# Kernel optimization log

Measured on AMD Instinct MI355X. Metric: run time of the kernel, lower is better.

The kernel has to match this reference:

```python
import jax, jax.numpy as jnp
import numpy as np

B, S, D_IN, D_OUT, H = 4, 2048, 2048, 2048, 16
HD = D_OUT // H  # head_dim = 128


def setup_inputs() -> dict:
    key = jax.random.key(0)
    ks = jax.random.split(key, 5)
    s = 0.02
    return {
        "x": jax.random.normal(ks[0], (B, S, D_IN), dtype=jnp.float32),
        "W_q": jax.random.normal(ks[1], (D_IN, D_OUT), dtype=jnp.float32) * s,
        "W_k": jax.random.normal(ks[2], (D_IN, D_OUT), dtype=jnp.float32) * s,
        "W_v": jax.random.normal(ks[3], (D_IN, D_OUT), dtype=jnp.float32) * s,
        "W_o": jax.random.normal(ks[4], (D_OUT, D_OUT), dtype=jnp.float32) * s,
        "b_o": jnp.zeros((D_OUT,), dtype=jnp.float32),
    }


def reference(x, W_q, W_k, W_v, W_o, b_o):
    b, n, _ = x.shape
    # projections (qkv_bias=False), split into heads: [b, h, n, hd]
    q = (x @ W_q).reshape(b, n, H, HD).transpose(0, 2, 1, 3)
    k = (x @ W_k).reshape(b, n, H, HD).transpose(0, 2, 1, 3)
    v = (x @ W_v).reshape(b, n, H, HD).transpose(0, 2, 1, 3)
    # scores [b, h, n, n], causal mask (triu, diagonal=1) applied BEFORE scaling
    scores = jnp.einsum("bhqd,bhkd->bhqk", q, k)
    causal = jnp.triu(jnp.ones((n, n), dtype=bool), k=1)
    scores = jnp.where(causal, -jnp.inf, scores)
    scale = jnp.asarray(HD, scores.dtype) ** 0.5
    attn = jax.nn.softmax(scores / scale, axis=-1)
    ctx = jnp.einsum("bhqk,bhkd->bhqd", attn, v)
    ctx = ctx.transpose(0, 2, 1, 3).reshape(b, n, D_OUT)
    return ctx @ W_o + b_o
```

## Files before the change

### kernel.cpp

```cpp
#include <hip/hip_runtime.h>
#include <hip/hip_bf16.h>
#include <math.h>

#define H_   16
#define S_   2048
#define D_   2048
#define HD_  128
#define B_   4
#define M_   8192

typedef __attribute__((ext_vector_type(8))) short short8;
typedef __attribute__((ext_vector_type(4))) short short4v;
typedef __attribute__((ext_vector_type(4))) float f32x4;

__device__ __forceinline__ short f2bf(float f) {
  unsigned u = __float_as_uint(f);
  u += 0x7fff + ((u >> 16) & 1);
  return (short)(u >> 16);
}

__device__ __forceinline__ unsigned pk2(float a, float b) {
  __hip_bfloat162 h = __float22bfloat162_rn(float2{a, b});
  union { __hip_bfloat162 h2; unsigned u; } c;
  c.h2 = h;
  return c.u;
}

__device__ __forceinline__ void async16(const void* g, void* l) {
  __builtin_amdgcn_global_load_lds(
      (const __attribute__((address_space(1))) void*)g,
      (__attribute__((address_space(3))) void*)l, 16, 0, 0);
}

__global__ void k_cvtx(const float* __restrict__ x, short* __restrict__ o, int n4) {
  const int i = blockIdx.x * 256 + threadIdx.x;
  if (i >= n4) return;
  const float4 f = ((const float4*)x)[i];
  short4v s;
  s.x = f2bf(f.x); s.y = f2bf(f.y); s.z = f2bf(f.z); s.w = f2bf(f.w);
  ((short4v*)o)[i] = s;
}

__global__ void k_wtrans(const float* __restrict__ W, short* __restrict__ Wt) {
  __shared__ float t[32][33];
  const int n0 = blockIdx.x << 5, k0 = blockIdx.y << 5;
  const int tc = threadIdx.x & 31, tr = threadIdx.x >> 5;
#pragma unroll
  for (int i = 0; i < 32; i += 8)
    t[tr + i][tc] = W[(size_t)(k0 + tr + i) * D_ + n0 + tc];
  __syncthreads();
#pragma unroll
  for (int i = 0; i < 32; i += 8)
    Wt[(size_t)(n0 + tr + i) * D_ + k0 + tc] = f2bf(t[tc][tr + i]);
}

template <int MODE>
__global__ __launch_bounds__(256)
void k_gemm_bt(const short* __restrict__ A, const short* __restrict__ Bt,
               void* __restrict__ C0, void* __restrict__ C1, void* __restrict__ C2,
               const float* __restrict__ bias, int M, int N, int K) {
  __shared__ __align__(16) short As[2][128 * 32];
  __shared__ __align__(16) short Bs[2][128 * 32];
  const int tid = threadIdx.x;
  const int lane = tid & 63;
  const int wave = tid >> 6;
  const int ln = lane & 15, lq = lane >> 4;
  const int bm = blockIdx.y << 7;
  const int bn = blockIdx.x << 7;
  const int wm = (wave >> 1) << 6;
  const int wn = (wave & 1) << 6;

  f32x4 acc[4][4];
#pragma unroll
  for (int i = 0; i < 4; i++)
#pragma unroll
    for (int j = 0; j < 4; j++) acc[i][j] = (f32x4)0.0f;

  const int srow = wave * 16 + (lane >> 2);
  const int scol = (lane & 3) * 8;
  const short* Ag = A  + (size_t)(bm + srow) * K + scol;
  const short* Bg = Bt + (size_t)(bn + srow) * K + scol;
  const int w16 = wave * 16 * 32;
  const int w16b = (64 + wave * 16) * 32;

  const int niter = K >> 5;
  async16(Ag, &As[0][w16]);
  async16(Ag + (size_t)64 * K, &As[0][w16b]);
  async16(Bg, &Bs[0][w16]);
  async16(Bg + (size_t)64 * K, &Bs[0][w16b]);

#pragma unroll 1
  for (int it = 0; it < niter; it++) {
    const int cur = it & 1;
    __syncthreads();
    if (it + 1 < niter) {
      const int k0 = (it + 1) << 5;
      async16(Ag + k0, &As[cur ^ 1][w16]);
      async16(Ag + (size_t)64 * K + k0, &As[cur ^ 1][w16b]);
      async16(Bg + k0, &Bs[cur ^ 1][w16]);
      async16(Bg + (size_t)64 * K + k0, &Bs[cur ^ 1][w16b]);
    }

    short8 af[4], bf[4];
#pragma unroll
    for (int i = 0; i < 4; i++)
      af[i] = *(const short8*)(&As[cur][(wm + i * 16 + ln) * 32 + lq * 8]);
#pragma unroll
    for (int i = 0; i < 4; i++)
      bf[i] = *(const short8*)(&Bs[cur][(wn + i * 16 + ln) * 32 + lq * 8]);
#pragma unroll
    for (int mi = 0; mi < 4; mi++)
#pragma unroll
      for (int ni = 0; ni < 4; ni++)
        acc[mi][ni] = __builtin_amdgcn_mfma_f32_16x16x32_bf16(
            af[mi], bf[ni], acc[mi][ni], 0, 0, 0);
  }

  if (MODE == 0) {
    const int proj = bn >> 11;
    const int cb = bn & 2047;
    if (proj < 2) {
      short* C = (short*)(proj == 0 ? C0 : C1);
#pragma unroll
      for (int mi = 0; mi < 4; mi++)
#pragma unroll
        for (int ni = 0; ni < 4; ni++) {
          const int col = cb + wn + ni * 16 + ln;
          const int h = col >> 7, d = col & 127;
#pragma unroll
          for (int r = 0; r < 4; r++) {
            const int row = bm + wm + mi * 16 + lq * 4 + r;
            const int bb = row >> 11, s = row & 2047;
            C[((size_t)((bb * H_ + h) * S_ + s)) * HD_ + d] = f2bf(acc[mi][ni][r]);
          }
        }
    } else {
      short* C = (short*)C2;
#pragma unroll
      for (int mi = 0; mi < 4; mi++)
#pragma unroll
        for (int ni = 0; ni < 4; ni++) {
          const int col = cb + wn + ni * 16 + ln;
          const int h = col >> 7, d = col & 127;
          const int row0 = bm + wm + mi * 16 + lq * 4;
          const int bb = row0 >> 11, s = row0 & 2047;
          short4v pk;
#pragma unroll
          for (int r = 0; r < 4; r++) pk[r] = f2bf(acc[mi][ni][r]);
          *(short4v*)(C + ((size_t)((bb * H_ + h) * HD_ + d)) * S_ + s) = pk;
        }
    }
  } else {
    float* C = (float*)C0;
#pragma unroll
    for (int mi = 0; mi < 4; mi++)
#pragma unroll
      for (int ni = 0; ni < 4; ni++) {
        const int col = bn + wn + ni * 16 + ln;
        const float bv = bias[col];
#pragma unroll
        for (int r = 0; r < 4; r++) {
          const int row = bm + wm + mi * 16 + lq * 4 + r;
          C[(size_t)row * N + col] = acc[mi][ni][r] + bv;
        }
      }
  }
}

__global__ __launch_bounds__(256)
void k_flash(const short* __restrict__ Q, const short* __restrict__ K,
             const short* __restrict__ Vt, short* __restrict__ ctx) {
  __shared__ __align__(16) short Ks[2][64 * 128];
  __shared__ __align__(16) short Vs[2][128 * 64];
  __shared__ __align__(16) short Ps[4 * 32 * 64];

  const int tid = threadIdx.x, lane = tid & 63, w = tid >> 6;
  const int ln = lane & 15, lq = lane >> 4;
  const int bh = blockIdx.x & 63;
  const int pr = blockIdx.x >> 6;
  const int b = bh >> 4, h = bh & 15;
  const short* Qp = Q  + (size_t)bh * S_ * HD_;
  const short* Kp = K  + (size_t)bh * S_ * HD_;
  const short* Vp = Vt + (size_t)bh * HD_ * S_;

  const float sc = 0.08838834764831845f * 1.4426950408889634f;
  const int lx = ln & 7;

  int koff[4], voff[4];
#pragma unroll
  for (int it = 0; it < 4; it++) {
    const int kr = w * 16 + it * 4 + (lane >> 4);
    koff[it] = kr * HD_ + (((lane & 15) ^ (kr & 7)) * 8);
    const int vr = w * 32 + it * 8 + (lane >> 3);
    voff[it] = vr * S_ + (((lane & 7) ^ (vr & 7)) * 8);
  }

#pragma unroll 1
  for (int pass = 0; pass < 2; pass++) {
    const int qb = pass ? (15 - pr) : pr;
    const int q0 = qb << 7;
    const int qw = q0 + w * 32;
    const int nkt = qb * 2 + 2;

    short8 qf[2][4];
#pragma unroll
    for (int nt = 0; nt < 2; nt++)
#pragma unroll
      for (int c = 0; c < 4; c++)
        qf[nt][c] = *(const short8*)(Qp + (size_t)(qw + nt * 16 + ln) * HD_ + c * 32 + lq * 8);

    f32x4 acc[8][2];
#pragma unroll
    for (int t = 0; t < 8; t++) { acc[t][0] = (f32x4)0.0f; acc[t][1] = (f32x4)0.0f; }
    float l_i[2] = {0.0f, 0.0f};

    __syncthreads();
#pragma unroll
    for (int it = 0; it < 4; it++) {
      async16(Kp + koff[it], &Ks[0][(w * 16 + it * 4) * 128]);
      async16(Vp + voff[it], &Vs[0][(w * 32 + it * 8) * 64]);
    }

#pragma unroll 1
    for (int kt = 0; kt < nkt; kt++) {
      const int k0 = kt << 6;
      const int cur = kt & 1;
      __syncthreads();
      if (kt + 1 < nkt) {
        const int nk0 = (kt + 1) << 6;
        const int nb = cur ^ 1;
#pragma unroll
        for (int it = 0; it < 4; it++) {
          async16(Kp + (size_t)nk0 * HD_ + koff[it], &Ks[nb][(w * 16 + it * 4) * 128]);
          async16(Vp + nk0 + voff[it],               &Vs[nb][(w * 32 + it * 8) * 64]);
        }
      }

      if (k0 <= qw + 31) {
        const short* KsC = Ks[cur];
        const short* VsC = Vs[cur];
        short* Pw = Ps + w * 32 * 64;
        const bool dg = (k0 + 63 > qw);

#pragma unroll
        for (int mt = 0; mt < 4; mt++) {
          f32x4 s0 = (f32x4)0.0f, s1 = (f32x4)0.0f;
#pragma unroll
          for (int c = 0; c < 4; c++) {
            short8 kf = *(const short8*)(KsC + (mt * 16 + ln) * 128 + (((4 * c + lq) ^ lx) * 8));
            s0 = __builtin_amdgcn_mfma_f32_16x16x32_bf16(kf, qf[0][c], s0, 0, 0, 0);
            s1 = __builtin_amdgcn_mfma_f32_16x16x32_bf16(kf, qf[1][c], s1, 0, 0, 0);
          }
          if (dg) {
#pragma unroll
            for (int r = 0; r < 4; r++) {
              const int kv = k0 + mt * 16 + lq * 4 + r;
              if (kv > qw + ln)      s0[r] = -INFINITY; else s0[r] *= sc;
              if (kv > qw + 16 + ln) s1[r] = -INFINITY; else s1[r] *= sc;
            }
          } else {
#pragma unroll
            for (int r = 0; r < 4; r++) { s0[r] *= sc; s1[r] *= sc; }
          }
#pragma unroll
          for (int r = 0; r < 4; r++) {
            s0[r] = exp2f(s0[r]); l_i[0] += s0[r];
            s1[r] = exp2f(s1[r]); l_i[1] += s1[r];
          }
          const int swc = (2 * mt + (lq >> 1)) ^ lx;
          const int po = swc * 8 + (lq & 1) * 4;
          *(uint2*)(Pw + ln * 64 + po)        = uint2{pk2(s0[0], s0[1]), pk2(s0[2], s0[3])};
          *(uint2*)(Pw + (16 + ln) * 64 + po) = uint2{pk2(s1[0], s1[1]), pk2(s1[2], s1[3])};
        }
        __asm__ volatile("s_waitcnt lgkmcnt(0)" ::: "memory");

#pragma unroll
        for (int c = 0; c < 2; c++) {
          const int swr = ((4 * c + lq) ^ lx) * 8;
          short8 pf0 = *(const short8*)(Pw + ln * 64 + swr);
          short8 pf1 = *(const short8*)(Pw + (16 + ln) * 64 + swr);
#pragma unroll
          for (int t = 0; t < 8; t++) {
            short8 vf = *(const short8*)(VsC + (t * 16 + ln) * 64 + swr);
            acc[t][0] = __builtin_amdgcn_mfma_f32_16x16x32_bf16(vf, pf0, acc[t][0], 0, 0, 0);
            acc[t][1] = __builtin_amdgcn_mfma_f32_16x16x32_bf16(vf, pf1, acc[t][1], 0, 0, 0);
          }
        }
      }
    }

#pragma unroll
    for (int o = 16; o < 64; o <<= 1) {
      l_i[0] += __shfl_xor(l_i[0], o, 64);
      l_i[1] += __shfl_xor(l_i[1], o, 64);
    }
    const float il[2] = {1.0f / l_i[0], 1.0f / l_i[1]};

#pragma unroll
    for (int t = 0; t < 8; t++)
#pragma unroll
      for (int nt = 0; nt < 2; nt++) {
        const int q = qw + nt * 16 + ln;
        const int d = t * 16 + lq * 4;
        uint2 o2 = {pk2(acc[t][nt][0] * il[nt], acc[t][nt][1] * il[nt]),
                    pk2(acc[t][nt][2] * il[nt], acc[t][nt][3] * il[nt])};
        *(uint2*)(ctx + ((size_t)(b * S_ + q)) * D_ + h * HD_ + d) = o2;
      }
  }
}

extern "C" void kernel_launch(void* const* d_in, const int* in_sizes, int n_in,
                              void* d_out, int out_size, void* d_ws, size_t ws_size,
                              hipStream_t stream) {
  const float* x  = (const float*)d_in[0];
  const float* Wq = (const float*)d_in[1];
  const float* Wk = (const float*)d_in[2];
  const float* Wv = (const float*)d_in[3];
  const float* Wo = (const float*)d_in[4];
  const float* bo = (const float*)d_in[5];
  float* out = (float*)d_out;

  char* ws = (char*)d_ws;
  const size_t SZ_X = (size_t)M_ * D_ * sizeof(short);
  const size_t SZ_W = (size_t)D_ * D_ * sizeof(short);
  short* xb  = (short*)(ws);
  short* Wqt = (short*)(ws + SZ_X);
  short* Wkt = (short*)(ws + SZ_X + SZ_W);
  short* Wvt = (short*)(ws + SZ_X + 2 * SZ_W);
  short* Wot = (short*)(ws + SZ_X + 3 * SZ_W);
  short* Qb  = (short*)(ws + SZ_X + 4 * SZ_W);
  short* Kb  = (short*)(ws + 2 * SZ_X + 4 * SZ_W);
  short* Vtb = (short*)(ws + 3 * SZ_X + 4 * SZ_W);
  short* ctx = (short*)(ws + 4 * SZ_X + 4 * SZ_W);

  k_cvtx<<<M_ * D_ / 4 / 256, 256, 0, stream>>>(x, xb, M_ * D_ / 4);
  dim3 tg(D_ / 32, D_ / 32);
  k_wtrans<<<tg, 256, 0, stream>>>(Wq, Wqt);
  k_wtrans<<<tg, 256, 0, stream>>>(Wk, Wkt);
  k_wtrans<<<tg, 256, 0, stream>>>(Wv, Wvt);
  k_wtrans<<<tg, 256, 0, stream>>>(Wo, Wot);

  dim3 gq(3 * D_ / 128, M_ / 128);
  k_gemm_bt<0><<<gq, 256, 0, stream>>>(xb, Wqt, Qb, Kb, Vtb, nullptr, M_, 3 * D_, D_);

  k_flash<<<8 * 64, 256, 0, stream>>>(Qb, Kb, Vtb, ctx);

  dim3 go(D_ / 128, M_ / 128);
  k_gemm_bt<1><<<go, 256, 0, stream>>>(ctx, Wot, out, nullptr, nullptr, bo, M_, D_, D_);
}
```

Baseline: 668.9 us.

## Replace 128x128 GEMM with 256x256 8-wave tile, swizzled LDS and ping-pong pipeline

Replaces the projection and output GEMM kernel with a 256x256 block tile, 512 threads (8 waves), and K-step 64. Each wave computes 128x64 in four quadrants. LDS is XOR-swizzled to avoid bank conflicts. Global-to-LDS async loads are staged across quadrants with explicit waitcnt/barrier scheduling and s_setprio around the MFMA bursts. This raises arithmetic intensity per byte loaded and overlaps memory with compute, at the cost of heavy register use (128 accumulator floats per lane) and fragile hand-written synchronisation.

```diff
diff --git a/kernel.cpp b/kernel.cpp
--- a/kernel.cpp
+++ b/kernel.cpp
@@ -54,66 +54,153 @@
     Wt[(size_t)(n0 + tr + i) * D_ + k0 + tc] = f2bf(t[tc][tr + i]);
 }
 
+
+#define GBAR() asm volatile("s_barrier" ::: "memory")
+#define WLG0()                                          \
+  do {                                                  \
+    asm volatile("s_waitcnt lgkmcnt(0)" ::: "memory");  \
+    __builtin_amdgcn_sched_barrier(0);                  \
+  } while (0)
+
+#define STG_A(b, mh, t)                                           \
+  do {                                                            \
+    const size_t o_ = (size_t)(t) * 64 + (size_t)(mh) * 64 * K;   \
+    async16(Ag0 + o_, &As[b][mh][ldst]);                          \
+    async16(Ag1 + o_, &As[b][mh][4096 + ldst]);                   \
+  } while (0)
+
+#define STG_B(b, nh, t)                                           \
+  do {                                                            \
+    const size_t o_ = (size_t)(t) * 64 + (size_t)(nh) * 32 * K;   \
+    async16(Bg0 + o_, &Bs[b][nh][ldst]);                          \
+    async16(Bg1 + o_, &Bs[b][nh][4096 + ldst]);                   \
+  } while (0)
+
+#define LDS_A(b, mh)                                                     \
+  do {                                                                   \
+    const char* a_ = (const char*)&As[b][mh][0];                         \
+    _Pragma("unroll") for (int mi_ = 0; mi_ < 4; ++mi_) {                \
+      af[mi_ * 2]     = *(const short8*)(a_ + rdA + mi_ * 2048 + cc0);   \
+      af[mi_ * 2 + 1] = *(const short8*)(a_ + rdA + mi_ * 2048 + cc1);   \
+    }                                                                    \
+  } while (0)
+
+#define LDS_B(b, nh, BF)                                                 \
+  do {                                                                   \
+    const char* b_ = (const char*)&Bs[b][nh][0];                         \
+    _Pragma("unroll") for (int ni_ = 0; ni_ < 2; ++ni_) {                \
+      BF[ni_ * 2]     = *(const short8*)(b_ + rdB + ni_ * 2048 + cc0);   \
+      BF[ni_ * 2 + 1] = *(const short8*)(b_ + rdB + ni_ * 2048 + cc1);   \
+    }                                                                    \
+  } while (0)
+
+#define QUAD(mh, nh, BF)                                                   \
+  do {                                                                     \
+    __builtin_amdgcn_s_setprio(1);                                         \
+    _Pragma("unroll") for (int mi_ = 0; mi_ < 4; ++mi_)                    \
+    _Pragma("unroll") for (int ni_ = 0; ni_ < 2; ++ni_) {                  \
+      acc[(mh) * 4 + mi_][(nh) * 2 + ni_] =                                \
+          __builtin_amdgcn_mfma_f32_16x16x32_bf16(                         \
+              af[mi_ * 2], BF[ni_ * 2],                                    \
+              acc[(mh) * 4 + mi_][(nh) * 2 + ni_], 0, 0, 0);               \
+      acc[(mh) * 4 + mi_][(nh) * 2 + ni_] =                                \
+          __builtin_amdgcn_mfma_f32_16x16x32_bf16(                         \
+              af[mi_ * 2 + 1], BF[ni_ * 2 + 1],                            \
+              acc[(mh) * 4 + mi_][(nh) * 2 + ni_], 0, 0, 0);               \
+    }                                                                      \
+    __builtin_amdgcn_s_setprio(0);                                         \
+  } while (0)
+
+#define TILE(T, b)                                                  \
+  do {                                                              \
+                           \
+    LDS_A(b, 0);                                                    \
+    LDS_B(b, 0, bf0);                                               \
+    if ((T) + 1 < NT) STG_A((b) ^ 1, 1, (T) + 1);                   \
+    asm volatile("s_waitcnt lgkmcnt(8)" ::: "memory");              \
+    GBAR();                                                         \
+    WLG0();                                                         \
+    QUAD(0, 0, bf0);                                                \
+    GBAR();                                                         \
+                           \
+    LDS_B(b, 1, bf1);                                               \
+    if ((T) + 2 < NT) STG_A(b, 0, (T) + 2);                         \
+    GBAR();                                                         \
+    WLG0();                                                         \
+    QUAD(0, 1, bf1);                                                \
+    GBAR();                                                         \
+                           \
+    LDS_A(b, 1);                                                    \
+    if ((T) + 2 < NT) STG_B(b, 0, (T) + 2);                         \
+    GBAR();                                                         \
+    WLG0();                                                         \
+    QUAD(1, 0, bf0);                                                \
+    GBAR();                                                         \
+                           \
+    if ((T) + 2 < NT) STG_B(b, 1, (T) + 2);                         \
+    if ((T) + 2 < NT)                                               \
+      asm volatile("s_waitcnt vmcnt(6)" ::: "memory");              \
+    else if ((T) + 1 < NT)                                          \
+      asm volatile("s_waitcnt vmcnt(0)" ::: "memory");              \
+    GBAR();                                                         \
+    QUAD(1, 1, bf1);                                                \
+    GBAR();                                                         \
+  } while (0)
+
 template <int MODE>
-__global__ __launch_bounds__(256)
-void k_gemm_bt(const short* __restrict__ A, const short* __restrict__ Bt,
+__global__ __launch_bounds__(512, 2)
+void k_gemm256(const short* __restrict__ A, const short* __restrict__ Bt,
                void* __restrict__ C0, void* __restrict__ C1, void* __restrict__ C2,
                const float* __restrict__ bias, int M, int N, int K) {
-  __shared__ __align__(16) short As[2][128 * 32];
-  __shared__ __align__(16) short Bs[2][128 * 32];
+  __shared__ __align__(16) short As[2][2][8192];
+  __shared__ __align__(16) short Bs[2][2][8192];
   const int tid = threadIdx.x;
   const int lane = tid & 63;
   const int wave = tid >> 6;
   const int ln = lane & 15, lq = lane >> 4;
-  const int bm = blockIdx.y << 7;
-  const int bn = blockIdx.x << 7;
-  const int wm = (wave >> 1) << 6;
-  const int wn = (wave & 1) << 6;
-
-  f32x4 acc[4][4];
-#pragma unroll
-  for (int i = 0; i < 4; i++)
+  const int wr = wave >> 2, wc = wave & 3;
+  const int bn = blockIdx.x << 8;
+  const int bm = blockIdx.y << 8;
+  const int NT = K >> 6;
+
+  const int r0 = wave * 8 + (lane >> 3);
+  const int k0 = ((lane & 7) ^ ((lane >> 3) & 7)) << 3;
+  const short* Ag0 = A  + (size_t)(bm + r0) * K + k0;
+  const short* Ag1 = A  + (size_t)(bm + 128 + r0) * K + k0;
+  const short* Bg0 = Bt + (size_t)(bn + ((r0 >> 5) << 6) + (r0 & 31)) * K + k0;
+  const short* Bg1 = Bt + (size_t)(bn + (((r0 >> 5) + 2) << 6) + (r0 & 31)) * K + k0;
+  const int ldst = wave * 512;
+
+  const int swz = (ln & 7) << 4;
+  const int rdA = (wr * 64 + ln) * 128;
+  const int rdB = (wc * 32 + ln) * 128;
+  const int cc0 = (lq * 16) ^ swz;
+  const int cc1 = (64 + lq * 16) ^ swz;
+
+  f32x4 acc[8][4];
+#pragma unroll
+  for (int i = 0; i < 8; i++)
 #pragma unroll
     for (int j = 0; j < 4; j++) acc[i][j] = (f32x4)0.0f;
 
-  const int srow = wave * 16 + (lane >> 2);
-  const int scol = (lane & 3) * 8;
-  const short* Ag = A  + (size_t)(bm + srow) * K + scol;
-  const short* Bg = Bt + (size_t)(bn + srow) * K + scol;
-  const int w16 = wave * 16 * 32;
-  const int w16b = (64 + wave * 16) * 32;
-
-  const int niter = K >> 5;
-  async16(Ag, &As[0][w16]);
-  async16(Ag + (size_t)64 * K, &As[0][w16b]);
-  async16(Bg, &Bs[0][w16]);
-  async16(Bg + (size_t)64 * K, &Bs[0][w16b]);
+  STG_A(0, 0, 0);
+  STG_B(0, 0, 0);
+  STG_B(0, 1, 0);
+  STG_A(0, 1, 0);
+  asm volatile("s_waitcnt vmcnt(4)" ::: "memory");
+  STG_A(1, 0, 1);
+  STG_B(1, 0, 1);
+  STG_B(1, 1, 1);
+  asm volatile("s_waitcnt vmcnt(6)" ::: "memory");
+  GBAR();
+
+  short8 af[8];
+  short8 bf0[4], bf1[4];
 
 #pragma unroll 1
-  for (int it = 0; it < niter; it++) {
-    const int cur = it & 1;
-    __syncthreads();
-    if (it + 1 < niter) {
-      const int k0 = (it + 1) << 5;
-      async16(Ag + k0, &As[cur ^ 1][w16]);
-      async16(Ag + (size_t)64 * K + k0, &As[cur ^ 1][w16b]);
-      async16(Bg + k0, &Bs[cur ^ 1][w16]);
-      async16(Bg + (size_t)64 * K + k0, &Bs[cur ^ 1][w16b]);
-    }
-
-    short8 af[4], bf[4];
-#pragma unroll
-    for (int i = 0; i < 4; i++)
-      af[i] = *(const short8*)(&As[cur][(wm + i * 16 + ln) * 32 + lq * 8]);
-#pragma unroll
-    for (int i = 0; i < 4; i++)
-      bf[i] = *(const short8*)(&Bs[cur][(wn + i * 16 + ln) * 32 + lq * 8]);
-#pragma unroll
-    for (int mi = 0; mi < 4; mi++)
-#pragma unroll
-      for (int ni = 0; ni < 4; ni++)
-        acc[mi][ni] = __builtin_amdgcn_mfma_f32_16x16x32_bf16(
-            af[mi], bf[ni], acc[mi][ni], 0, 0, 0);
+  for (int T = 0; T < NT; T += 2) {
+    TILE(T, 0);
+    TILE(T + 1, 1);
   }
 
   if (MODE == 0) {
@@ -122,14 +209,14 @@
     if (proj < 2) {
       short* C = (short*)(proj == 0 ? C0 : C1);
 #pragma unroll
-      for (int mi = 0; mi < 4; mi++)
+      for (int mi = 0; mi < 8; mi++)
 #pragma unroll
         for (int ni = 0; ni < 4; ni++) {
-          const int col = cb + wn + ni * 16 + ln;
+          const int col = cb + wc * 64 + ni * 16 + ln;
           const int h = col >> 7, d = col & 127;
 #pragma unroll
           for (int r = 0; r < 4; r++) {
-            const int row = bm + wm + mi * 16 + lq * 4 + r;
+            const int row = bm + wr * 128 + mi * 16 + lq * 4 + r;
             const int bb = row >> 11, s = row & 2047;
             C[((size_t)((bb * H_ + h) * S_ + s)) * HD_ + d] = f2bf(acc[mi][ni][r]);
           }
@@ -137,12 +224,12 @@
     } else {
       short* C = (short*)C2;
 #pragma unroll
-      for (int mi = 0; mi < 4; mi++)
+      for (int mi = 0; mi < 8; mi++)
 #pragma unroll
         for (int ni = 0; ni < 4; ni++) {
-          const int col = cb + wn + ni * 16 + ln;
+          const int col = cb + wc * 64 + ni * 16 + ln;
           const int h = col >> 7, d = col & 127;
-          const int row0 = bm + wm + mi * 16 + lq * 4;
+          const int row0 = bm + wr * 128 + mi * 16 + lq * 4;
           const int bb = row0 >> 11, s = row0 & 2047;
           short4v pk;
 #pragma unroll
@@ -153,14 +240,14 @@
   } else {
     float* C = (float*)C0;
 #pragma unroll
-    for (int mi = 0; mi < 4; mi++)
+    for (int mi = 0; mi < 8; mi++)
 #pragma unroll
       for (int ni = 0; ni < 4; ni++) {
-        const int col = bn + wn + ni * 16 + ln;
+        const int col = bn + wc * 64 + ni * 16 + ln;
         const float bv = bias[col];
 #pragma unroll
         for (int r = 0; r < 4; r++) {
-          const int row = bm + wm + mi * 16 + lq * 4 + r;
+          const int row = bm + wr * 128 + mi * 16 + lq * 4 + r;
           C[(size_t)row * N + col] = acc[mi][ni][r] + bv;
         }
       }
@@ -340,11 +427,11 @@
   k_wtrans<<<tg, 256, 0, stream>>>(Wv, Wvt);
   k_wtrans<<<tg, 256, 0, stream>>>(Wo, Wot);
 
-  dim3 gq(3 * D_ / 128, M_ / 128);
-  k_gemm_bt<0><<<gq, 256, 0, stream>>>(xb, Wqt, Qb, Kb, Vtb, nullptr, M_, 3 * D_, D_);
+  dim3 gq(3 * D_ / 256, M_ / 256);
+  k_gemm256<0><<<gq, 512, 0, stream>>>(xb, Wqt, Qb, Kb, Vtb, nullptr, M_, 3 * D_, D_);
 
   k_flash<<<8 * 64, 256, 0, stream>>>(Qb, Kb, Vtb, ctx);
 
-  dim3 go(D_ / 128, M_ / 128);
-  k_gemm_bt<1><<<go, 256, 0, stream>>>(ctx, Wot, out, nullptr, nullptr, bo, M_, D_, D_);
-}
+  dim3 go(D_ / 256, M_ / 256);
+  k_gemm256<1><<<go, 512, 0, stream>>>(ctx, Wot, out, nullptr, nullptr, bo, M_, D_, D_);
+}
```

New measurement: 611.9 us. 1.09x faster.
